# Kernel optimization log

Hardware: AMD Instinct MI355X
Metric: run time of the kernel (lower is better)

The kernel has to match this reference:

```python
import jax, jax.numpy as jnp
import numpy as np

NUM_EXPERTS = 16
HIDDEN = 1024
INTERMEDIATE = 4096
TOTAL_TOKENS = 32768  # 2048 tokens per expert


def setup_inputs() -> dict:
    key = jax.random.key(0)
    k1, k2, k3 = jax.random.split(key, 3)
    hidden_states = jax.random.normal(k1, (TOTAL_TOKENS, HIDDEN), dtype=jnp.float32)
    gate_up_proj = jax.random.normal(k2, (NUM_EXPERTS, HIDDEN, 2 * INTERMEDIATE), dtype=jnp.float32)
    down_proj = jax.random.normal(k3, (NUM_EXPERTS, INTERMEDIATE, HIDDEN), dtype=jnp.float32)
    return {"hidden_states": hidden_states, "gate_up_proj": gate_up_proj, "down_proj": down_proj}


def reference(hidden_states, gate_up_proj, down_proj):
    E, H = gate_up_proj.shape[0], gate_up_proj.shape[1]
    # (E, T, H): tokens pre-grouped by expert, as in the torch module's reshape
    x = hidden_states.reshape(E, -1, H)
    # batched expert GEMM: (E,T,H) @ (E,H,2I) -> (E,T,2I)
    gate_up = jnp.einsum('eth,ehf->etf', x, gate_up_proj)
    gate, up = jnp.split(gate_up, 2, axis=-1)
    gated = up * jax.nn.silu(gate)  # SwiGLU
    # down projection: (E,T,I) @ (E,I,H) -> (E,T,H)
    out = jnp.einsum('eti,eih->eth', gated, down_proj)
    return out.reshape(-1, H)
```

## Files before the change

### kernel.cpp

```cpp
#include <hip/hip_runtime.h>
#include <hip/hip_bf16.h>
#include <cstdint>
#include <cstddef>

#define NE  16
#define HD  1024
#define ID  4096
#define TPE 2048
#define TOKENS 32768

typedef __attribute__((ext_vector_type(8))) short short8;
typedef __attribute__((ext_vector_type(4))) float f32x4;
typedef __attribute__((ext_vector_type(4))) unsigned short u16x4;
typedef __attribute__((ext_vector_type(8))) unsigned short u16x8;

static __device__ __forceinline__ unsigned short f2b(float f) {
    __bf16 h = (__bf16)f;
    return __builtin_bit_cast(unsigned short, h);
}

#define GLOAD16(gsrc, ldsbase)                                                  \
    __builtin_amdgcn_global_load_lds(                                           \
        (const __attribute__((address_space(1))) unsigned int*)(gsrc),          \
        (__attribute__((address_space(3))) unsigned int*)(ldsbase), 16, 0, 0)

#define MFMA16(a, b, c) __builtin_amdgcn_mfma_f32_16x16x32_bf16((a), (b), (c), 0, 0, 0)

static __device__ __forceinline__ int xcd_swz(int bid, int nwg) {
    int q = nwg >> 3;
    return (bid & 7) * q + (bid >> 3);
}

__global__ void k_f2b(const float* __restrict__ src, unsigned short* __restrict__ dst, int n4)
{
    int i = blockIdx.x * blockDim.x + threadIdx.x;
    int stride = gridDim.x * blockDim.x;
    for (; i < n4; i += stride) {
        float4 v = *(const float4*)(src + (size_t)i * 4);
        u16x4 b = { f2b(v.x), f2b(v.y), f2b(v.z), f2b(v.w) };
        *(u16x4*)(dst + (size_t)i * 4) = b;
    }
}

__global__ __launch_bounds__(256) void k_transpose(const float* __restrict__ src,
                                                   unsigned short* __restrict__ dst,
                                                   int K, int N, int e0)
{
    __shared__ unsigned short LT[64][72];
    const int t  = threadIdx.x;
    const int eL = blockIdx.z;
    const float* s = src + (size_t)(e0 + eL) * K * N
                         + (size_t)(blockIdx.y * 64) * N + blockIdx.x * 64;
    unsigned short* d = dst + (size_t)eL * N * K
                            + (size_t)(blockIdx.x * 64) * K + blockIdx.y * 64;

    const int ct = t & 15;
    const int rt = t >> 4;
    float4 v0 = *(const float4*)(s + (size_t)(rt * 4 + 0) * N + ct * 4);
    float4 v1 = *(const float4*)(s + (size_t)(rt * 4 + 1) * N + ct * 4);
    float4 v2 = *(const float4*)(s + (size_t)(rt * 4 + 2) * N + ct * 4);
    float4 v3 = *(const float4*)(s + (size_t)(rt * 4 + 3) * N + ct * 4);
    {
        u16x4 w0 = { f2b(v0.x), f2b(v1.x), f2b(v2.x), f2b(v3.x) };
        u16x4 w1 = { f2b(v0.y), f2b(v1.y), f2b(v2.y), f2b(v3.y) };
        u16x4 w2 = { f2b(v0.z), f2b(v1.z), f2b(v2.z), f2b(v3.z) };
        u16x4 w3 = { f2b(v0.w), f2b(v1.w), f2b(v2.w), f2b(v3.w) };
        *(u16x4*)&LT[ct * 4 + 0][rt * 4] = w0;
        *(u16x4*)&LT[ct * 4 + 1][rt * 4] = w1;
        *(u16x4*)&LT[ct * 4 + 2][rt * 4] = w2;
        *(u16x4*)&LT[ct * 4 + 3][rt * 4] = w3;
    }
    __syncthreads();
    #pragma unroll
    for (int i = 0; i < 2; ++i) {
        int n  = i * 32 + (t >> 3);
        int k8 = (t & 7) * 8;
        u16x8 v = *(const u16x8*)&LT[n][k8];
        *(u16x8*)(d + (size_t)n * K + k8) = v;
    }
}

__global__ __launch_bounds__(512, 2) void k_gemm1(const unsigned short* __restrict__ hsB,
                                                  const unsigned short* __restrict__ gupT,
                                                  unsigned short* __restrict__ gated,
                                                  int e0)
{
    __shared__ unsigned short As[2][256 * 64];
    __shared__ unsigned short Bs[2][256 * 64];
    const int NT = HD / 64;

    const int s    = xcd_swz(blockIdx.x, gridDim.x);
    const int bx   = s & 31;
    const int by   = (s >> 5) & 7;
    const int eL   = s >> 8;

    const int t    = threadIdx.x;
    const int lane = t & 63;
    const int w    = t >> 6;
    const int wr   = w >> 2;
    const int wc   = w & 3;
    const int e    = e0 + eL;
    const int n0g  = bx * 128;
    const int m0   = by * 256;

    const unsigned short* gA  = hsB  + (size_t)(e * TPE + m0) * HD;
    const unsigned short* gBt = gupT + (size_t)eL * (2 * ID) * HD;

    f32x4 acc[8][4];
    #pragma unroll
    for (int i = 0; i < 8; ++i)
        #pragma unroll
        for (int j = 0; j < 4; ++j)
            acc[i][j] = f32x4{0.f, 0.f, 0.f, 0.f};

    auto STAGE = [&](int buf, int kt) {
        #pragma unroll
        for (int i = 0; i < 4; ++i) {
            int idx = i * 512 + t;
            int row = idx >> 3, sl = idx & 7;
            GLOAD16(gA + (size_t)row * HD + kt * 64 + ((sl ^ (row & 7)) << 3),
                    &As[buf][(size_t)(i * 512 + (t & ~63)) * 8]);
        }
        #pragma unroll
        for (int i = 0; i < 4; ++i) {
            int idx = i * 512 + t;
            int c = idx >> 3, sl = idx & 7;
            int g = c >> 5;
            int grow = ((g & 1) ? ID : 0) + n0g + ((g >> 1) << 5) + (c & 31);
            GLOAD16(gBt + (size_t)grow * HD + kt * 64 + ((sl ^ (c & 7)) << 3),
                    &Bs[buf][(size_t)(i * 512 + (t & ~63)) * 8]);
        }
    };

    STAGE(0, 0);
    STAGE(1, 1);

    for (int kt = 0; kt < NT; ++kt) {
        const int cur = kt & 1;
        const unsigned short* Ab = &As[cur][0];
        const unsigned short* Bb = &Bs[cur][0];

        if (kt < NT - 1) { asm volatile("s_waitcnt vmcnt(8)" ::: "memory"); }
        else             { asm volatile("s_waitcnt vmcnt(0)" ::: "memory"); }
        __builtin_amdgcn_s_barrier();

        short8 av[8], bv[4];
        #pragma unroll
        for (int fm = 0; fm < 8; ++fm) {
            int row = wr * 128 + fm * 16 + (lane & 15);
            int sl  = (lane >> 4);
            av[fm] = *(const short8*)&Ab[row * 64 + ((sl ^ (row & 7)) << 3)];
        }
        #pragma unroll
        for (int fn = 0; fn < 4; ++fn) {
            int c  = wc * 64 + fn * 16 + (lane & 15);
            int sl = (lane >> 4);
            bv[fn] = *(const short8*)&Bb[c * 64 + ((sl ^ (c & 7)) << 3)];
        }
        __builtin_amdgcn_s_setprio(1);
        #pragma unroll
        for (int fm = 0; fm < 8; ++fm)
            #pragma unroll
            for (int fn = 0; fn < 4; ++fn)
                acc[fm][fn] = MFMA16(av[fm], bv[fn], acc[fm][fn]);
        __builtin_amdgcn_s_setprio(0);

        short8 av1[8], bv1[4];
        #pragma unroll
        for (int fm = 0; fm < 8; ++fm) {
            int row = wr * 128 + fm * 16 + (lane & 15);
            int sl  = 4 + (lane >> 4);
            av1[fm] = *(const short8*)&Ab[row * 64 + ((sl ^ (row & 7)) << 3)];
        }
        #pragma unroll
        for (int fn = 0; fn < 4; ++fn) {
            int c  = wc * 64 + fn * 16 + (lane & 15);
            int sl = 4 + (lane >> 4);
            bv1[fn] = *(const short8*)&Bb[c * 64 + ((sl ^ (c & 7)) << 3)];
        }
        asm volatile("s_waitcnt lgkmcnt(0)" ::: "memory");
        __builtin_amdgcn_sched_barrier(0);
        __builtin_amdgcn_s_barrier();
        if (kt + 2 < NT)
            STAGE(cur, kt + 2);
        __builtin_amdgcn_s_setprio(1);
        #pragma unroll
        for (int fm = 0; fm < 8; ++fm)
            #pragma unroll
            for (int fn = 0; fn < 4; ++fn)
                acc[fm][fn] = MFMA16(av1[fm], bv1[fn], acc[fm][fn]);
        __builtin_amdgcn_s_setprio(0);
    }
    asm volatile("s_waitcnt vmcnt(0)" ::: "memory");

    unsigned short* g0 = gated + ((size_t)eL * TPE + m0) * ID;
    const int rq = (lane >> 4) << 2;
    const int cl = lane & 15;
    #pragma unroll
    for (int fm = 0; fm < 8; ++fm) {
        #pragma unroll
        for (int fp = 0; fp < 2; ++fp) {
            f32x4 g = acc[fm][fp];
            f32x4 u = acc[fm][fp + 2];
            #pragma unroll
            for (int r = 0; r < 4; ++r) {
                float gv  = g[r];
                float val = u[r] * gv / (1.0f + __expf(-gv));
                int row = wr * 128 + fm * 16 + rq + r;
                int col = n0g + wc * 32 + fp * 16 + cl;
                g0[(size_t)row * ID + col] = f2b(val);
            }
        }
    }
}

__global__ __launch_bounds__(512, 2) void k_gemm2(const unsigned short* __restrict__ gated,
                                                  const unsigned short* __restrict__ dwnT,
                                                  float* __restrict__ out,
                                                  int e0)
{
    __shared__ unsigned short As[2][256 * 64];
    __shared__ unsigned short Bs[2][256 * 64];
    const int NT = ID / 64;

    const int s    = xcd_swz(blockIdx.x, gridDim.x);
    const int bx   = s & 3;
    const int by   = (s >> 2) & 7;
    const int eL   = s >> 5;

    const int t    = threadIdx.x;
    const int lane = t & 63;
    const int w    = t >> 6;
    const int wr   = w >> 2;
    const int wc   = w & 3;
    const int e    = e0 + eL;
    const int n0   = bx * 256;
    const int m0   = by * 256;

    const unsigned short* gA  = gated + ((size_t)eL * TPE + m0) * ID;
    const unsigned short* gBt = dwnT  + (size_t)eL * HD * ID;

    f32x4 acc[8][4];
    #pragma unroll
    for (int i = 0; i < 8; ++i)
        #pragma unroll
        for (int j = 0; j < 4; ++j)
            acc[i][j] = f32x4{0.f, 0.f, 0.f, 0.f};

    auto STAGE = [&](int buf, int kt) {
        #pragma unroll
        for (int i = 0; i < 4; ++i) {
            int idx = i * 512 + t;
            int row = idx >> 3, sl = idx & 7;
            GLOAD16(gA + (size_t)row * ID + kt * 64 + ((sl ^ (row & 7)) << 3),
                    &As[buf][(size_t)(i * 512 + (t & ~63)) * 8]);
        }
        #pragma unroll
        for (int i = 0; i < 4; ++i) {
            int idx = i * 512 + t;
            int c = idx >> 3, sl = idx & 7;
            GLOAD16(gBt + (size_t)(n0 + c) * ID + kt * 64 + ((sl ^ (c & 7)) << 3),
                    &Bs[buf][(size_t)(i * 512 + (t & ~63)) * 8]);
        }
    };

    STAGE(0, 0);
    STAGE(1, 1);

    for (int kt = 0; kt < NT; ++kt) {
        const int cur = kt & 1;
        const unsigned short* Ab = &As[cur][0];
        const unsigned short* Bb = &Bs[cur][0];

        if (kt < NT - 1) { asm volatile("s_waitcnt vmcnt(8)" ::: "memory"); }
        else             { asm volatile("s_waitcnt vmcnt(0)" ::: "memory"); }
        __builtin_amdgcn_s_barrier();

        short8 av[8], bv[4];
        #pragma unroll
        for (int fm = 0; fm < 8; ++fm) {
            int row = wr * 128 + fm * 16 + (lane & 15);
            int sl  = (lane >> 4);
            av[fm] = *(const short8*)&Ab[row * 64 + ((sl ^ (row & 7)) << 3)];
        }
        #pragma unroll
        for (int fn = 0; fn < 4; ++fn) {
            int c  = wc * 64 + fn * 16 + (lane & 15);
            int sl = (lane >> 4);
            bv[fn] = *(const short8*)&Bb[c * 64 + ((sl ^ (c & 7)) << 3)];
        }
        __builtin_amdgcn_s_setprio(1);
        #pragma unroll
        for (int fm = 0; fm < 8; ++fm)
            #pragma unroll
            for (int fn = 0; fn < 4; ++fn)
                acc[fm][fn] = MFMA16(av[fm], bv[fn], acc[fm][fn]);
        __builtin_amdgcn_s_setprio(0);

        short8 av1[8], bv1[4];
        #pragma unroll
        for (int fm = 0; fm < 8; ++fm) {
            int row = wr * 128 + fm * 16 + (lane & 15);
            int sl  = 4 + (lane >> 4);
            av1[fm] = *(const short8*)&Ab[row * 64 + ((sl ^ (row & 7)) << 3)];
        }
        #pragma unroll
        for (int fn = 0; fn < 4; ++fn) {
            int c  = wc * 64 + fn * 16 + (lane & 15);
            int sl = 4 + (lane >> 4);
            bv1[fn] = *(const short8*)&Bb[c * 64 + ((sl ^ (c & 7)) << 3)];
        }
        asm volatile("s_waitcnt lgkmcnt(0)" ::: "memory");
        __builtin_amdgcn_sched_barrier(0);
        __builtin_amdgcn_s_barrier();
        if (kt + 2 < NT)
            STAGE(cur, kt + 2);
        __builtin_amdgcn_s_setprio(1);
        #pragma unroll
        for (int fm = 0; fm < 8; ++fm)
            #pragma unroll
            for (int fn = 0; fn < 4; ++fn)
                acc[fm][fn] = MFMA16(av1[fm], bv1[fn], acc[fm][fn]);
        __builtin_amdgcn_s_setprio(0);
    }
    asm volatile("s_waitcnt vmcnt(0)" ::: "memory");

    float* o0 = out + (size_t)(e * TPE + m0) * HD;
    const int rq = (lane >> 4) << 2;
    const int cl = lane & 15;
    #pragma unroll
    for (int fm = 0; fm < 8; ++fm) {
        #pragma unroll
        for (int fn = 0; fn < 4; ++fn) {
            #pragma unroll
            for (int r = 0; r < 4; ++r) {
                int row = wr * 128 + fm * 16 + rq + r;
                int col = n0 + wc * 64 + fn * 16 + cl;
                o0[(size_t)row * HD + col] = acc[fm][fn][r];
            }
        }
    }
}

extern "C" void kernel_launch(void* const* d_in, const int* in_sizes, int n_in,
                              void* d_out, int out_size, void* d_ws, size_t ws_size,
                              hipStream_t stream)
{
    (void)in_sizes; (void)n_in; (void)out_size;
    const float* hs  = (const float*)d_in[0];
    const float* gup = (const float*)d_in[1];
    const float* dwn = (const float*)d_in[2];
    float* out = (float*)d_out;

    const size_t SZ_HSB   = (size_t)TOKENS * HD * 2;
    const size_t SZ_GUPT  = (size_t)2 * ID * HD * 2;
    const size_t SZ_DWNT  = (size_t)HD * ID * 2;
    const size_t SZ_GATED = (size_t)TPE * ID * 2;
    const size_t perExp   = SZ_GUPT + SZ_DWNT + SZ_GATED;

    int G = (ws_size > SZ_HSB) ? (int)((ws_size - SZ_HSB) / perExp) : 1;
    if (G < 1) G = 1;
    if (G > NE) G = NE;

    unsigned short* hsB   = (unsigned short*)d_ws;
    unsigned short* gupT  = (unsigned short*)((char*)d_ws + SZ_HSB);
    unsigned short* dwnT  = (unsigned short*)((char*)d_ws + SZ_HSB + (size_t)G * SZ_GUPT);
    unsigned short* gated = (unsigned short*)((char*)d_ws + SZ_HSB + (size_t)G * (SZ_GUPT + SZ_DWNT));

    k_f2b<<<2048, 256, 0, stream>>>(hs, hsB, TOKENS * HD / 4);

    for (int e0 = 0; e0 < NE; e0 += G) {
        int ne = NE - e0;
        if (ne > G) ne = G;
        k_transpose<<<dim3((2 * ID) / 64, HD / 64, ne), 256, 0, stream>>>(gup, gupT, HD, 2 * ID, e0);
        k_transpose<<<dim3(HD / 64, ID / 64, ne), 256, 0, stream>>>(dwn, dwnT, ID, HD, e0);
        k_gemm1<<<256 * ne, 512, 0, stream>>>(hsB, gupT, gated, e0);
        k_gemm2<<<32 * ne, 512, 0, stream>>>(gated, dwnT, out, e0);
    }
}
```

Measured before the change: 1.155 ms.

## Switch GEMMs to 32x32x16 MFMA tiles and drop XCD block swizzle

```diff
diff --git a/kernel.cpp b/kernel.cpp
--- a/kernel.cpp
+++ b/kernel.cpp
@@ -10,7 +10,7 @@
 #define TOKENS 32768
 
 typedef __attribute__((ext_vector_type(8))) short short8;
-typedef __attribute__((ext_vector_type(4))) float f32x4;
+typedef __attribute__((ext_vector_type(16))) float f32x16;
 typedef __attribute__((ext_vector_type(4))) unsigned short u16x4;
 typedef __attribute__((ext_vector_type(8))) unsigned short u16x8;
 
@@ -24,12 +24,7 @@
         (const __attribute__((address_space(1))) unsigned int*)(gsrc),          \
         (__attribute__((address_space(3))) unsigned int*)(ldsbase), 16, 0, 0)
 
-#define MFMA16(a, b, c) __builtin_amdgcn_mfma_f32_16x16x32_bf16((a), (b), (c), 0, 0, 0)
-
-static __device__ __forceinline__ int xcd_swz(int bid, int nwg) {
-    int q = nwg >> 3;
-    return (bid & 7) * q + (bid >> 3);
-}
+#define MFMA32(a, b, c) __builtin_amdgcn_mfma_f32_32x32x16_bf16((a), (b), (c), 0, 0, 0)
 
 __global__ void k_f2b(const float* __restrict__ src, unsigned short* __restrict__ dst, int n4)
 {
@@ -89,29 +84,27 @@
     __shared__ unsigned short Bs[2][256 * 64];
     const int NT = HD / 64;
 
-    const int s    = xcd_swz(blockIdx.x, gridDim.x);
-    const int bx   = s & 31;
-    const int by   = (s >> 5) & 7;
-    const int eL   = s >> 8;
-
     const int t    = threadIdx.x;
     const int lane = t & 63;
     const int w    = t >> 6;
     const int wr   = w >> 2;
     const int wc   = w & 3;
+    const int eL   = blockIdx.z;
     const int e    = e0 + eL;
-    const int n0g  = bx * 128;
-    const int m0   = by * 256;
+    const int n0g  = blockIdx.x * 128;
+    const int m0   = blockIdx.y * 256;
 
     const unsigned short* gA  = hsB  + (size_t)(e * TPE + m0) * HD;
     const unsigned short* gBt = gupT + (size_t)eL * (2 * ID) * HD;
 
-    f32x4 acc[8][4];
-    #pragma unroll
-    for (int i = 0; i < 8; ++i)
-        #pragma unroll
-        for (int j = 0; j < 4; ++j)
-            acc[i][j] = f32x4{0.f, 0.f, 0.f, 0.f};
+    f32x16 acc[4][2];
+    #pragma unroll
+    for (int i = 0; i < 4; ++i)
+        #pragma unroll
+        for (int j = 0; j < 2; ++j)
+            #pragma unroll
+            for (int q = 0; q < 16; ++q)
+                acc[i][j][q] = 0.f;
 
     auto STAGE = [&](int buf, int kt) {
         #pragma unroll
@@ -146,38 +139,48 @@
 
         short8 av[8], bv[4];
         #pragma unroll
-        for (int fm = 0; fm < 8; ++fm) {
-            int row = wr * 128 + fm * 16 + (lane & 15);
-            int sl  = (lane >> 4);
-            av[fm] = *(const short8*)&Ab[row * 64 + ((sl ^ (row & 7)) << 3)];
-        }
-        #pragma unroll
-        for (int fn = 0; fn < 4; ++fn) {
-            int c  = wc * 64 + fn * 16 + (lane & 15);
-            int sl = (lane >> 4);
-            bv[fn] = *(const short8*)&Bb[c * 64 + ((sl ^ (c & 7)) << 3)];
-        }
+        for (int mt = 0; mt < 4; ++mt)
+            #pragma unroll
+            for (int j = 0; j < 2; ++j) {
+                int row = wr * 128 + mt * 32 + (lane & 31);
+                int sl  = j * 2 + (lane >> 5);
+                av[mt * 2 + j] = *(const short8*)&Ab[row * 64 + ((sl ^ (row & 7)) << 3)];
+            }
+        #pragma unroll
+        for (int nt = 0; nt < 2; ++nt)
+            #pragma unroll
+            for (int j = 0; j < 2; ++j) {
+                int c  = wc * 64 + nt * 32 + (lane & 31);
+                int sl = j * 2 + (lane >> 5);
+                bv[nt * 2 + j] = *(const short8*)&Bb[c * 64 + ((sl ^ (c & 7)) << 3)];
+            }
         __builtin_amdgcn_s_setprio(1);
         #pragma unroll
-        for (int fm = 0; fm < 8; ++fm)
-            #pragma unroll
-            for (int fn = 0; fn < 4; ++fn)
-                acc[fm][fn] = MFMA16(av[fm], bv[fn], acc[fm][fn]);
+        for (int mt = 0; mt < 4; ++mt)
+            #pragma unroll
+            for (int nt = 0; nt < 2; ++nt)
+                #pragma unroll
+                for (int j = 0; j < 2; ++j)
+                    acc[mt][nt] = MFMA32(av[mt * 2 + j], bv[nt * 2 + j], acc[mt][nt]);
         __builtin_amdgcn_s_setprio(0);
 
         short8 av1[8], bv1[4];
         #pragma unroll
-        for (int fm = 0; fm < 8; ++fm) {
-            int row = wr * 128 + fm * 16 + (lane & 15);
-            int sl  = 4 + (lane >> 4);
-            av1[fm] = *(const short8*)&Ab[row * 64 + ((sl ^ (row & 7)) << 3)];
-        }
-        #pragma unroll
-        for (int fn = 0; fn < 4; ++fn) {
-            int c  = wc * 64 + fn * 16 + (lane & 15);
-            int sl = 4 + (lane >> 4);
-            bv1[fn] = *(const short8*)&Bb[c * 64 + ((sl ^ (c & 7)) << 3)];
-        }
+        for (int mt = 0; mt < 4; ++mt)
+            #pragma unroll
+            for (int j = 0; j < 2; ++j) {
+                int row = wr * 128 + mt * 32 + (lane & 31);
+                int sl  = 4 + j * 2 + (lane >> 5);
+                av1[mt * 2 + j] = *(const short8*)&Ab[row * 64 + ((sl ^ (row & 7)) << 3)];
+            }
+        #pragma unroll
+        for (int nt = 0; nt < 2; ++nt)
+            #pragma unroll
+            for (int j = 0; j < 2; ++j) {
+                int c  = wc * 64 + nt * 32 + (lane & 31);
+                int sl = 4 + j * 2 + (lane >> 5);
+                bv1[nt * 2 + j] = *(const short8*)&Bb[c * 64 + ((sl ^ (c & 7)) << 3)];
+            }
         asm volatile("s_waitcnt lgkmcnt(0)" ::: "memory");
         __builtin_amdgcn_sched_barrier(0);
         __builtin_amdgcn_s_barrier();
@@ -185,29 +188,30 @@
             STAGE(cur, kt + 2);
         __builtin_amdgcn_s_setprio(1);
         #pragma unroll
-        for (int fm = 0; fm < 8; ++fm)
-            #pragma unroll
-            for (int fn = 0; fn < 4; ++fn)
-                acc[fm][fn] = MFMA16(av1[fm], bv1[fn], acc[fm][fn]);
+        for (int mt = 0; mt < 4; ++mt)
+            #pragma unroll
+            for (int nt = 0; nt < 2; ++nt)
+                #pragma unroll
+                for (int j = 0; j < 2; ++j)
+                    acc[mt][nt] = MFMA32(av1[mt * 2 + j], bv1[nt * 2 + j], acc[mt][nt]);
         __builtin_amdgcn_s_setprio(0);
     }
     asm volatile("s_waitcnt vmcnt(0)" ::: "memory");
 
     unsigned short* g0 = gated + ((size_t)eL * TPE + m0) * ID;
-    const int rq = (lane >> 4) << 2;
-    const int cl = lane & 15;
-    #pragma unroll
-    for (int fm = 0; fm < 8; ++fm) {
-        #pragma unroll
-        for (int fp = 0; fp < 2; ++fp) {
-            f32x4 g = acc[fm][fp];
-            f32x4 u = acc[fm][fp + 2];
+    const int cl = lane & 31;
+    const int rq = (lane >> 5) << 2;
+    #pragma unroll
+    for (int mt = 0; mt < 4; ++mt) {
+        #pragma unroll
+        for (int q = 0; q < 4; ++q) {
             #pragma unroll
             for (int r = 0; r < 4; ++r) {
-                float gv  = g[r];
-                float val = u[r] * gv / (1.0f + __expf(-gv));
-                int row = wr * 128 + fm * 16 + rq + r;
-                int col = n0g + wc * 32 + fp * 16 + cl;
+                float gv = acc[mt][0][q * 4 + r];
+                float uv = acc[mt][1][q * 4 + r];
+                float val = uv * gv / (1.0f + __expf(-gv));
+                int row = wr * 128 + mt * 32 + rq + q * 8 + r;
+                int col = n0g + wc * 32 + cl;
                 g0[(size_t)row * ID + col] = f2b(val);
             }
         }
@@ -222,30 +226,28 @@
     __shared__ unsigned short As[2][256 * 64];
     __shared__ unsigned short Bs[2][256 * 64];
     const int NT = ID / 64;
-
-    const int s    = xcd_swz(blockIdx.x, gridDim.x);
-    const int bx   = s & 3;
-    const int by   = (s >> 2) & 7;
-    const int eL   = s >> 5;
 
     const int t    = threadIdx.x;
     const int lane = t & 63;
     const int w    = t >> 6;
     const int wr   = w >> 2;
     const int wc   = w & 3;
+    const int eL   = blockIdx.z;
     const int e    = e0 + eL;
-    const int n0   = bx * 256;
-    const int m0   = by * 256;
+    const int n0   = blockIdx.x * 256;
+    const int m0   = blockIdx.y * 256;
 
     const unsigned short* gA  = gated + ((size_t)eL * TPE + m0) * ID;
     const unsigned short* gBt = dwnT  + (size_t)eL * HD * ID;
 
-    f32x4 acc[8][4];
-    #pragma unroll
-    for (int i = 0; i < 8; ++i)
-        #pragma unroll
-        for (int j = 0; j < 4; ++j)
-            acc[i][j] = f32x4{0.f, 0.f, 0.f, 0.f};
+    f32x16 acc[4][2];
+    #pragma unroll
+    for (int i = 0; i < 4; ++i)
+        #pragma unroll
+        for (int j = 0; j < 2; ++j)
+            #pragma unroll
+            for (int q = 0; q < 16; ++q)
+                acc[i][j][q] = 0.f;
 
     auto STAGE = [&](int buf, int kt) {
         #pragma unroll
@@ -278,38 +280,48 @@
 
         short8 av[8], bv[4];
         #pragma unroll
-        for (int fm = 0; fm < 8; ++fm) {
-            int row = wr * 128 + fm * 16 + (lane & 15);
-            int sl  = (lane >> 4);
-            av[fm] = *(const short8*)&Ab[row * 64 + ((sl ^ (row & 7)) << 3)];
-        }
-        #pragma unroll
-        for (int fn = 0; fn < 4; ++fn) {
-            int c  = wc * 64 + fn * 16 + (lane & 15);
-            int sl = (lane >> 4);
-            bv[fn] = *(const short8*)&Bb[c * 64 + ((sl ^ (c & 7)) << 3)];
-        }
+        for (int mt = 0; mt < 4; ++mt)
+            #pragma unroll
+            for (int j = 0; j < 2; ++j) {
+                int row = wr * 128 + mt * 32 + (lane & 31);
+                int sl  = j * 2 + (lane >> 5);
+                av[mt * 2 + j] = *(const short8*)&Ab[row * 64 + ((sl ^ (row & 7)) << 3)];
+            }
+        #pragma unroll
+        for (int nt = 0; nt < 2; ++nt)
+            #pragma unroll
+            for (int j = 0; j < 2; ++j) {
+                int c  = wc * 64 + nt * 32 + (lane & 31);
+                int sl = j * 2 + (lane >> 5);
+                bv[nt * 2 + j] = *(const short8*)&Bb[c * 64 + ((sl ^ (c & 7)) << 3)];
+            }
         __builtin_amdgcn_s_setprio(1);
         #pragma unroll
-        for (int fm = 0; fm < 8; ++fm)
-            #pragma unroll
-            for (int fn = 0; fn < 4; ++fn)
-                acc[fm][fn] = MFMA16(av[fm], bv[fn], acc[fm][fn]);
+        for (int mt = 0; mt < 4; ++mt)
+            #pragma unroll
+            for (int nt = 0; nt < 2; ++nt)
+                #pragma unroll
+                for (int j = 0; j < 2; ++j)
+                    acc[mt][nt] = MFMA32(av[mt * 2 + j], bv[nt * 2 + j], acc[mt][nt]);
         __builtin_amdgcn_s_setprio(0);
 
         short8 av1[8], bv1[4];
         #pragma unroll
-        for (int fm = 0; fm < 8; ++fm) {
-            int row = wr * 128 + fm * 16 + (lane & 15);
-            int sl  = 4 + (lane >> 4);
-            av1[fm] = *(const short8*)&Ab[row * 64 + ((sl ^ (row & 7)) << 3)];
-        }
-        #pragma unroll
-        for (int fn = 0; fn < 4; ++fn) {
-            int c  = wc * 64 + fn * 16 + (lane & 15);
-            int sl = 4 + (lane >> 4);
-            bv1[fn] = *(const short8*)&Bb[c * 64 + ((sl ^ (c & 7)) << 3)];
-        }
+        for (int mt = 0; mt < 4; ++mt)
+            #pragma unroll
+            for (int j = 0; j < 2; ++j) {
+                int row = wr * 128 + mt * 32 + (lane & 31);
+                int sl  = 4 + j * 2 + (lane >> 5);
+                av1[mt * 2 + j] = *(const short8*)&Ab[row * 64 + ((sl ^ (row & 7)) << 3)];
+            }
+        #pragma unroll
+        for (int nt = 0; nt < 2; ++nt)
+            #pragma unroll
+            for (int j = 0; j < 2; ++j) {
+                int c  = wc * 64 + nt * 32 + (lane & 31);
+                int sl = 4 + j * 2 + (lane >> 5);
+                bv1[nt * 2 + j] = *(const short8*)&Bb[c * 64 + ((sl ^ (c & 7)) << 3)];
+            }
         asm volatile("s_waitcnt lgkmcnt(0)" ::: "memory");
         __builtin_amdgcn_sched_barrier(0);
         __builtin_amdgcn_s_barrier();
@@ -317,26 +329,31 @@
             STAGE(cur, kt + 2);
         __builtin_amdgcn_s_setprio(1);
         #pragma unroll
-        for (int fm = 0; fm < 8; ++fm)
-            #pragma unroll
-            for (int fn = 0; fn < 4; ++fn)
-                acc[fm][fn] = MFMA16(av1[fm], bv1[fn], acc[fm][fn]);
+        for (int mt = 0; mt < 4; ++mt)
+            #pragma unroll
+            for (int nt = 0; nt < 2; ++nt)
+                #pragma unroll
+                for (int j = 0; j < 2; ++j)
+                    acc[mt][nt] = MFMA32(av1[mt * 2 + j], bv1[nt * 2 + j], acc[mt][nt]);
         __builtin_amdgcn_s_setprio(0);
     }
     asm volatile("s_waitcnt vmcnt(0)" ::: "memory");
 
     float* o0 = out + (size_t)(e * TPE + m0) * HD;
-    const int rq = (lane >> 4) << 2;
-    const int cl = lane & 15;
-    #pragma unroll
-    for (int fm = 0; fm < 8; ++fm) {
-        #pragma unroll
-        for (int fn = 0; fn < 4; ++fn) {
-            #pragma unroll
-            for (int r = 0; r < 4; ++r) {
-                int row = wr * 128 + fm * 16 + rq + r;
-                int col = n0 + wc * 64 + fn * 16 + cl;
-                o0[(size_t)row * HD + col] = acc[fm][fn][r];
+    const int cl = lane & 31;
+    const int rq = (lane >> 5) << 2;
+    #pragma unroll
+    for (int mt = 0; mt < 4; ++mt) {
+        #pragma unroll
+        for (int nt = 0; nt < 2; ++nt) {
+            #pragma unroll
+            for (int q = 0; q < 4; ++q) {
+                #pragma unroll
+                for (int r = 0; r < 4; ++r) {
+                    int row = wr * 128 + mt * 32 + rq + q * 8 + r;
+                    int col = n0 + wc * 64 + nt * 32 + cl;
+                    o0[(size_t)row * HD + col] = acc[mt][nt][q * 4 + r];
+                }
             }
         }
     }
@@ -374,7 +391,7 @@
         if (ne > G) ne = G;
         k_transpose<<<dim3((2 * ID) / 64, HD / 64, ne), 256, 0, stream>>>(gup, gupT, HD, 2 * ID, e0);
         k_transpose<<<dim3(HD / 64, ID / 64, ne), 256, 0, stream>>>(dwn, dwnT, ID, HD, e0);
-        k_gemm1<<<256 * ne, 512, 0, stream>>>(hsB, gupT, gated, e0);
-        k_gemm2<<<32 * ne, 512, 0, stream>>>(gated, dwnT, out, e0);
-    }
-}
+        k_gemm1<<<dim3(ID / 128, TPE / 256, ne), 512, 0, stream>>>(hsB, gupT, gated, e0);
+        k_gemm2<<<dim3(HD / 256, TPE / 256, ne), 512, 0, stream>>>(gated, dwnT, out, e0);
+    }
+}
```

After: 1.207 ms. +4.5%, slower.
